# Kernel optimization log

Hardware: AMD Instinct MI355X
Metric: run time of the kernel (lower is better)

## Reference

```python
import jax, jax.numpy as jnp
import numpy as np

B, N_INST, H, W = 8, 64, 480, 480
EPS = 1e-12  # torch F.normalize eps


def setup_inputs() -> dict:
    key = jax.random.key(0)
    k1, k2, k3, k4, k5, k6 = jax.random.split(key, 6)
    # binary instance masks (output of connected-component labeling in the original)
    instance_masks = (jax.random.uniform(k1, (N_INST, H, W)) < 0.3).astype(jnp.float32)
    sample_ids = jax.random.randint(k2, (N_INST,), 0, B, dtype=jnp.int64)
    quaternion = jax.random.normal(k3, (B, 4, H, W), dtype=jnp.float32)
    scales = jax.random.normal(k4, (B, 3, H, W), dtype=jnp.float32)
    xy = jax.random.normal(k5, (B, 2, H, W), dtype=jnp.float32)
    z = jax.random.normal(k6, (B, H, W), dtype=jnp.float32)
    return {"instance_masks": instance_masks, "sample_ids": sample_ids,
            "quaternion": quaternion, "scales": scales, "xy": xy, "z": z}


def reference(instance_masks, sample_ids, quaternion, scales, xy, z):
    # instance_masks: [N,H,W] binary float; sample_ids: [N] in [0,B)
    mask_size = jnp.sum(instance_masks, axis=(-2, -1))  # [N]

    def masked_mean(d):  # d: [N,C,H,W] -> [N,C]
        return jnp.einsum('nhw,nchw->nc', instance_masks, d) / mask_size[:, None]

    # quaternion: masked mean then L2-normalize along channel dim
    q_agg = masked_mean(quaternion[sample_ids])                       # [N,4]
    q_agg = q_agg / jnp.maximum(jnp.linalg.norm(q_agg, axis=1, keepdims=True), EPS)
    # scales: masked mean
    s_agg = masked_mean(scales[sample_ids])                           # [N,3]
    # z: masked mean of [N,1,H,W] then exp
    z_agg = jnp.exp(masked_mean(z[sample_ids][:, None]))              # [N,1]
    # xy: masked dense map (passed on to hough voting downstream)
    xy_masked = instance_masks[:, None] * xy[sample_ids]              # [N,2,H,W]
    return q_agg, s_agg, z_agg, xy_masked
```

## Files before the change

### kernel.cpp

```cpp
#include <hip/hip_runtime.h>
#include <math.h>

#define HW      (480 * 480)
#define HW4     (HW / 4)
#define NINST   64
#define BPI     32
#define NV      9
#define THREADS 256

__global__ __launch_bounds__(THREADS) void agg_main(
    const float* __restrict__ masks,
    const int*   __restrict__ sids,
    const float* __restrict__ quat,
    const float* __restrict__ scales,
    const float* __restrict__ xy,
    const float* __restrict__ z,
    float*       __restrict__ out,
    float*       __restrict__ part)
{
    const int blk = blockIdx.x;
    const int n   = blk >> 5;
    const int b   = blk & (BPI - 1);
    const int tid = threadIdx.x;
    const int sid = sids[n];

    const float4* m4  = (const float4*)(masks + (size_t)n * HW);
    const float4* q0  = (const float4*)(quat  + ((size_t)sid * 4 + 0) * HW);
    const float4* q1  = (const float4*)(quat  + ((size_t)sid * 4 + 1) * HW);
    const float4* q2  = (const float4*)(quat  + ((size_t)sid * 4 + 2) * HW);
    const float4* q3  = (const float4*)(quat  + ((size_t)sid * 4 + 3) * HW);
    const float4* s0  = (const float4*)(scales + ((size_t)sid * 3 + 0) * HW);
    const float4* s1  = (const float4*)(scales + ((size_t)sid * 3 + 1) * HW);
    const float4* s2  = (const float4*)(scales + ((size_t)sid * 3 + 2) * HW);
    const float4* x0  = (const float4*)(xy    + ((size_t)sid * 2 + 0) * HW);
    const float4* x1  = (const float4*)(xy    + ((size_t)sid * 2 + 1) * HW);
    const float4* z0  = (const float4*)(z     + (size_t)sid * HW);
    float4* oxy0 = (float4*)(out + 512 + ((size_t)n * 2 + 0) * HW);
    float4* oxy1 = (float4*)(out + 512 + ((size_t)n * 2 + 1) * HW);

    float acc[NV];
#pragma unroll
    for (int v = 0; v < NV; ++v) acc[v] = 0.0f;

    for (int i = b * THREADS + tid; i < HW4; i += BPI * THREADS) {
        const float4 m = m4[i];

        const float4 a0 = x0[i];
        const float4 a1 = x1[i];
        oxy0[i] = make_float4(m.x * a0.x, m.y * a0.y, m.z * a0.z, m.w * a0.w);
        oxy1[i] = make_float4(m.x * a1.x, m.y * a1.y, m.z * a1.z, m.w * a1.w);

        acc[0] += (m.x + m.y) + (m.z + m.w);
        float4 t;
        t = q0[i]; acc[1] += m.x*t.x + m.y*t.y + m.z*t.z + m.w*t.w;
        t = q1[i]; acc[2] += m.x*t.x + m.y*t.y + m.z*t.z + m.w*t.w;
        t = q2[i]; acc[3] += m.x*t.x + m.y*t.y + m.z*t.z + m.w*t.w;
        t = q3[i]; acc[4] += m.x*t.x + m.y*t.y + m.z*t.z + m.w*t.w;
        t = s0[i]; acc[5] += m.x*t.x + m.y*t.y + m.z*t.z + m.w*t.w;
        t = s1[i]; acc[6] += m.x*t.x + m.y*t.y + m.z*t.z + m.w*t.w;
        t = s2[i]; acc[7] += m.x*t.x + m.y*t.y + m.z*t.z + m.w*t.w;
        t = z0[i]; acc[8] += m.x*t.x + m.y*t.y + m.z*t.z + m.w*t.w;
    }

    __shared__ float sred[4][NV];
    const int lane = tid & 63;
    const int wid  = tid >> 6;
#pragma unroll
    for (int v = 0; v < NV; ++v) {
        float val = acc[v];
#pragma unroll
        for (int off = 32; off > 0; off >>= 1)
            val += __shfl_down(val, off, 64);
        if (lane == 0) sred[wid][v] = val;
    }
    __syncthreads();
    if (tid < NV) {
        float s = sred[0][tid] + sred[1][tid] + sred[2][tid] + sred[3][tid];
        part[(size_t)blk * NV + tid] = s;
    }
}

__global__ __launch_bounds__(64) void agg_final(
    const float* __restrict__ part,
    float*       __restrict__ out)
{
    const int n = threadIdx.x;
    if (n >= NINST) return;

    float s[NV];
#pragma unroll
    for (int v = 0; v < NV; ++v) s[v] = 0.0f;
    for (int b = 0; b < BPI; ++b) {
        const float* p = part + ((size_t)n * BPI + b) * NV;
#pragma unroll
        for (int v = 0; v < NV; ++v) s[v] += p[v];
    }

    const float inv = 1.0f / s[0];
    const float q0 = s[1] * inv, q1 = s[2] * inv, q2 = s[3] * inv, q3 = s[4] * inv;
    const float norm = sqrtf(q0*q0 + q1*q1 + q2*q2 + q3*q3);
    const float d = fmaxf(norm, 1e-12f);
    out[n * 4 + 0] = q0 / d;
    out[n * 4 + 1] = q1 / d;
    out[n * 4 + 2] = q2 / d;
    out[n * 4 + 3] = q3 / d;

    out[256 + n * 3 + 0] = s[5] * inv;
    out[256 + n * 3 + 1] = s[6] * inv;
    out[256 + n * 3 + 2] = s[7] * inv;

    out[448 + n] = expf(s[8] * inv);
}

extern "C" void kernel_launch(void* const* d_in, const int* in_sizes, int n_in,
                              void* d_out, int out_size, void* d_ws, size_t ws_size,
                              hipStream_t stream) {
    const float* masks  = (const float*)d_in[0];
    const int*   sids   = (const int*)d_in[1];
    const float* quat   = (const float*)d_in[2];
    const float* scales = (const float*)d_in[3];
    const float* xy     = (const float*)d_in[4];
    const float* z      = (const float*)d_in[5];
    float* out  = (float*)d_out;
    float* part = (float*)d_ws;

    agg_main<<<NINST * BPI, THREADS, 0, stream>>>(masks, sids, quat, scales, xy, z, out, part);
    agg_final<<<1, 64, 0, stream>>>(part, out);
}
```

Baseline: 264.6 us.

## Reuse per-sample feature tiles across instances by iterating instances inside sample blocks

```diff
diff --git a/kernel.cpp b/kernel.cpp
--- a/kernel.cpp
+++ b/kernel.cpp
@@ -4,9 +4,10 @@
 #define HW      (480 * 480)
 #define HW4     (HW / 4)
 #define NINST   64
-#define BPI     32
+#define NB      8
 #define NV      9
 #define THREADS 256
+#define NCHUNK  (HW4 / THREADS)
 
 __global__ __launch_bounds__(THREADS) void agg_main(
     const float* __restrict__ masks,
@@ -18,48 +19,87 @@
     float*       __restrict__ out,
     float*       __restrict__ part)
 {
-    const int blk = blockIdx.x;
-    const int n   = blk >> 5;
-    const int b   = blk & (BPI - 1);
+    const int c   = blockIdx.x;
+    const int b   = blockIdx.y;
     const int tid = threadIdx.x;
-    const int sid = sids[n];
+    const int i   = c * THREADS + tid;
 
-    const float4* m4  = (const float4*)(masks + (size_t)n * HW);
-    const float4* q0  = (const float4*)(quat  + ((size_t)sid * 4 + 0) * HW);
-    const float4* q1  = (const float4*)(quat  + ((size_t)sid * 4 + 1) * HW);
-    const float4* q2  = (const float4*)(quat  + ((size_t)sid * 4 + 2) * HW);
-    const float4* q3  = (const float4*)(quat  + ((size_t)sid * 4 + 3) * HW);
-    const float4* s0  = (const float4*)(scales + ((size_t)sid * 3 + 0) * HW);
-    const float4* s1  = (const float4*)(scales + ((size_t)sid * 3 + 1) * HW);
-    const float4* s2  = (const float4*)(scales + ((size_t)sid * 3 + 2) * HW);
-    const float4* x0  = (const float4*)(xy    + ((size_t)sid * 2 + 0) * HW);
-    const float4* x1  = (const float4*)(xy    + ((size_t)sid * 2 + 1) * HW);
-    const float4* z0  = (const float4*)(z     + (size_t)sid * HW);
-    float4* oxy0 = (float4*)(out + 512 + ((size_t)n * 2 + 0) * HW);
-    float4* oxy1 = (float4*)(out + 512 + ((size_t)n * 2 + 1) * HW);
+    const float4* Q  = (const float4*)quat;
+    const float4* S  = (const float4*)scales;
+    const float4* X  = (const float4*)xy;
+    const float4* Z  = (const float4*)z;
+    const float4* M  = (const float4*)masks;
+    float4*       O  = (float4*)(out + 512);
 
-    float acc[NV];
+    const size_t qb = (size_t)b * 4 * HW4 + i;
+    const float4 vq0 = Q[qb + 0 * HW4];
+    const float4 vq1 = Q[qb + 1 * HW4];
+    const float4 vq2 = Q[qb + 2 * HW4];
+    const float4 vq3 = Q[qb + 3 * HW4];
+    const size_t sb = (size_t)b * 3 * HW4 + i;
+    const float4 vs0 = S[sb + 0 * HW4];
+    const float4 vs1 = S[sb + 1 * HW4];
+    const float4 vs2 = S[sb + 2 * HW4];
+    const size_t xb = (size_t)b * 2 * HW4 + i;
+    const float4 vx0 = X[xb + 0 * HW4];
+    const float4 vx1 = X[xb + 1 * HW4];
+    const float4 vz  = Z[(size_t)b * HW4 + i];
+
+    __shared__ float sred[4][NV];
+    const int lane = tid & 63;
+    const int wid  = tid >> 6;
+
+    for (int n = 0; n < NINST; ++n) {
+        if (sids[n] != b) continue;
+
+        const float4 m = M[(size_t)n * HW4 + i];
+
+        O[((size_t)n * 2 + 0) * HW4 + i] =
+            make_float4(m.x * vx0.x, m.y * vx0.y, m.z * vx0.z, m.w * vx0.w);
+        O[((size_t)n * 2 + 1) * HW4 + i] =
+            make_float4(m.x * vx1.x, m.y * vx1.y, m.z * vx1.z, m.w * vx1.w);
+
+        float vals[NV];
+        vals[0] = (m.x + m.y) + (m.z + m.w);
+        vals[1] = m.x*vq0.x + m.y*vq0.y + m.z*vq0.z + m.w*vq0.w;
+        vals[2] = m.x*vq1.x + m.y*vq1.y + m.z*vq1.z + m.w*vq1.w;
+        vals[3] = m.x*vq2.x + m.y*vq2.y + m.z*vq2.z + m.w*vq2.w;
+        vals[4] = m.x*vq3.x + m.y*vq3.y + m.z*vq3.z + m.w*vq3.w;
+        vals[5] = m.x*vs0.x + m.y*vs0.y + m.z*vs0.z + m.w*vs0.w;
+        vals[6] = m.x*vs1.x + m.y*vs1.y + m.z*vs1.z + m.w*vs1.w;
+        vals[7] = m.x*vs2.x + m.y*vs2.y + m.z*vs2.z + m.w*vs2.w;
+        vals[8] = m.x*vz.x  + m.y*vz.y  + m.z*vz.z  + m.w*vz.w;
+
 #pragma unroll
-    for (int v = 0; v < NV; ++v) acc[v] = 0.0f;
+        for (int v = 0; v < NV; ++v) {
+            float x = vals[v];
+#pragma unroll
+            for (int off = 32; off > 0; off >>= 1)
+                x += __shfl_down(x, off, 64);
+            if (lane == 0) sred[wid][v] = x;
+        }
+        __syncthreads();
+        if (tid < NV)
+            part[((size_t)n * NCHUNK + c) * NV + tid] =
+                (sred[0][tid] + sred[1][tid]) + (sred[2][tid] + sred[3][tid]);
+        __syncthreads();
+    }
+}
 
-    for (int i = b * THREADS + tid; i < HW4; i += BPI * THREADS) {
-        const float4 m = m4[i];
+__global__ __launch_bounds__(THREADS) void agg_final(
+    const float* __restrict__ part,
+    float*       __restrict__ out)
+{
+    const int n   = blockIdx.x;
+    const int tid = threadIdx.x;
 
-        const float4 a0 = x0[i];
-        const float4 a1 = x1[i];
-        oxy0[i] = make_float4(m.x * a0.x, m.y * a0.y, m.z * a0.z, m.w * a0.w);
-        oxy1[i] = make_float4(m.x * a1.x, m.y * a1.y, m.z * a1.z, m.w * a1.w);
-
-        acc[0] += (m.x + m.y) + (m.z + m.w);
-        float4 t;
-        t = q0[i]; acc[1] += m.x*t.x + m.y*t.y + m.z*t.z + m.w*t.w;
-        t = q1[i]; acc[2] += m.x*t.x + m.y*t.y + m.z*t.z + m.w*t.w;
-        t = q2[i]; acc[3] += m.x*t.x + m.y*t.y + m.z*t.z + m.w*t.w;
-        t = q3[i]; acc[4] += m.x*t.x + m.y*t.y + m.z*t.z + m.w*t.w;
-        t = s0[i]; acc[5] += m.x*t.x + m.y*t.y + m.z*t.z + m.w*t.w;
-        t = s1[i]; acc[6] += m.x*t.x + m.y*t.y + m.z*t.z + m.w*t.w;
-        t = s2[i]; acc[7] += m.x*t.x + m.y*t.y + m.z*t.z + m.w*t.w;
-        t = z0[i]; acc[8] += m.x*t.x + m.y*t.y + m.z*t.z + m.w*t.w;
+    float vals[NV];
+#pragma unroll
+    for (int v = 0; v < NV; ++v) vals[v] = 0.0f;
+    for (int c = tid; c < NCHUNK; c += THREADS) {
+        const float* p = part + ((size_t)n * NCHUNK + c) * NV;
+#pragma unroll
+        for (int v = 0; v < NV; ++v) vals[v] += p[v];
     }
 
     __shared__ float sred[4][NV];
@@ -67,49 +107,35 @@
     const int wid  = tid >> 6;
 #pragma unroll
     for (int v = 0; v < NV; ++v) {
-        float val = acc[v];
+        float x = vals[v];
 #pragma unroll
         for (int off = 32; off > 0; off >>= 1)
-            val += __shfl_down(val, off, 64);
-        if (lane == 0) sred[wid][v] = val;
+            x += __shfl_down(x, off, 64);
+        if (lane == 0) sred[wid][v] = x;
     }
     __syncthreads();
-    if (tid < NV) {
-        float s = sred[0][tid] + sred[1][tid] + sred[2][tid] + sred[3][tid];
-        part[(size_t)blk * NV + tid] = s;
+
+    if (tid == 0) {
+        float s[NV];
+#pragma unroll
+        for (int v = 0; v < NV; ++v)
+            s[v] = (sred[0][v] + sred[1][v]) + (sred[2][v] + sred[3][v]);
+
+        const float inv = 1.0f / s[0];
+        const float q0 = s[1] * inv, q1 = s[2] * inv, q2 = s[3] * inv, q3 = s[4] * inv;
+        const float norm = sqrtf(q0*q0 + q1*q1 + q2*q2 + q3*q3);
+        const float d = fmaxf(norm, 1e-12f);
+        out[n * 4 + 0] = q0 / d;
+        out[n * 4 + 1] = q1 / d;
+        out[n * 4 + 2] = q2 / d;
+        out[n * 4 + 3] = q3 / d;
+
+        out[256 + n * 3 + 0] = s[5] * inv;
+        out[256 + n * 3 + 1] = s[6] * inv;
+        out[256 + n * 3 + 2] = s[7] * inv;
+
+        out[448 + n] = expf(s[8] * inv);
     }
-}
-
-__global__ __launch_bounds__(64) void agg_final(
-    const float* __restrict__ part,
-    float*       __restrict__ out)
-{
-    const int n = threadIdx.x;
-    if (n >= NINST) return;
-
-    float s[NV];
-#pragma unroll
-    for (int v = 0; v < NV; ++v) s[v] = 0.0f;
-    for (int b = 0; b < BPI; ++b) {
-        const float* p = part + ((size_t)n * BPI + b) * NV;
-#pragma unroll
-        for (int v = 0; v < NV; ++v) s[v] += p[v];
-    }
-
-    const float inv = 1.0f / s[0];
-    const float q0 = s[1] * inv, q1 = s[2] * inv, q2 = s[3] * inv, q3 = s[4] * inv;
-    const float norm = sqrtf(q0*q0 + q1*q1 + q2*q2 + q3*q3);
-    const float d = fmaxf(norm, 1e-12f);
-    out[n * 4 + 0] = q0 / d;
-    out[n * 4 + 1] = q1 / d;
-    out[n * 4 + 2] = q2 / d;
-    out[n * 4 + 3] = q3 / d;
-
-    out[256 + n * 3 + 0] = s[5] * inv;
-    out[256 + n * 3 + 1] = s[6] * inv;
-    out[256 + n * 3 + 2] = s[7] * inv;
-
-    out[448 + n] = expf(s[8] * inv);
 }
 
 extern "C" void kernel_launch(void* const* d_in, const int* in_sizes, int n_in,
@@ -124,6 +150,7 @@
     float* out  = (float*)d_out;
     float* part = (float*)d_ws;
 
-    agg_main<<<NINST * BPI, THREADS, 0, stream>>>(masks, sids, quat, scales, xy, z, out, part);
-    agg_final<<<1, 64, 0, stream>>>(part, out);
+    dim3 grid(NCHUNK, NB);
+    agg_main<<<grid, THREADS, 0, stream>>>(masks, sids, quat, scales, xy, z, out, part);
+    agg_final<<<NINST, THREADS, 0, stream>>>(part, out);
 }
```

After: 245.6 us. 7.2% less time.
